# Performance work log

Measured on AMD Instinct MI355X. Metric: run time of the kernel, lower is better.

Reference implementation:

```python
import jax, jax.numpy as jnp
import numpy as np

EMBED_DIM = 1024
NUM_HEADS = 16
HEAD_DIM = EMBED_DIM // NUM_HEADS
SCALE = HEAD_DIM ** -0.5


def setup_inputs() -> dict:
    key = jax.random.key(0)
    ks = jax.random.split(key, 5)
    B, N, C = 4, 2048, EMBED_DIM
    s = C ** -0.5
    return {
        "x": jax.random.normal(ks[0], (B, N, C), dtype=jnp.float32),
        "w_qkv": jax.random.normal(ks[1], (C, 3 * C), dtype=jnp.float32) * s,
        "b_qkv": jnp.zeros((3 * C,), dtype=jnp.float32),
        "w_proj": jax.random.normal(ks[2], (C, C), dtype=jnp.float32) * s,
        "b_proj": jnp.zeros((C,), dtype=jnp.float32),
    }


def reference(x, w_qkv, b_qkv, w_proj, b_proj):
    B, N, C = x.shape
    H, D = NUM_HEADS, HEAD_DIM
    qkv = x @ w_qkv + b_qkv                      # (B, N, 3C)
    qkv = qkv.reshape(B, N, 3, H, D)
    qkv = jnp.transpose(qkv, (2, 0, 3, 1, 4))    # (3, B, H, N, D)
    q, k, v = qkv[0], qkv[1], qkv[2]
    attn = jnp.einsum('bhnd,bhmd->bhnm', q, k) * SCALE
    attn = jax.nn.softmax(attn, axis=-1)
    out = jnp.einsum('bhnm,bhmd->bhnd', attn, v)  # (B, H, N, D)
    out = jnp.transpose(out, (0, 2, 1, 3)).reshape(B, N, C)
    return out @ w_proj + b_proj
```

## Files before the change

### kernel.cpp

```cpp
#include <hip/hip_runtime.h>

typedef __attribute__((ext_vector_type(8))) short short8v;
typedef __attribute__((ext_vector_type(4))) short short4v;
typedef __attribute__((ext_vector_type(4))) float float4v;
typedef __attribute__((ext_vector_type(4))) unsigned short ushort4v;
typedef __attribute__((ext_vector_type(8))) unsigned short ushort8v;

#define GLOBAL_AS __attribute__((address_space(1)))
#define LDS_AS __attribute__((address_space(3)))

__device__ __forceinline__ void async_cp16(const void* g, void* l) {
  __builtin_amdgcn_global_load_lds((const GLOBAL_AS void*)g, (LDS_AS void*)l, 16, 0, 0);
}

__device__ __forceinline__ unsigned short f2bf(float f) {
  unsigned u = __float_as_uint(f);
  u += 0x7fffu + ((u >> 16) & 1u);
  return (unsigned short)(u >> 16);
}

#if defined(__HIP_DEVICE_COMPILE__)
#if __has_builtin(__builtin_amdgcn_exp2f)
#define EXP2F(x) __builtin_amdgcn_exp2f(x)
#else
#define EXP2F(x) exp2f(x)
#endif
#else
#define EXP2F(x) exp2f(x)
#endif

#if defined(__HIP_DEVICE_COMPILE__) && __has_builtin(__builtin_amdgcn_cvt_pk_bf16_f32)
typedef __attribute__((ext_vector_type(2))) __bf16 bf16x2v;
__device__ __forceinline__ unsigned pk_bf16(float a, float b) {
  bf16x2v r = __builtin_amdgcn_cvt_pk_bf16_f32(a, b);
  return __builtin_bit_cast(unsigned, r);
}
#else
__device__ __forceinline__ unsigned pk_bf16(float a, float b) {
  return (unsigned)f2bf(a) | ((unsigned)f2bf(b) << 16);
}
#endif

#define MFMA_QK(a, b, c) __builtin_amdgcn_mfma_f32_16x16x32_bf16(a, b, c, 0, 0, 0)


__global__ __launch_bounds__(256) void cvt_f32_bf16(const float* __restrict__ src,
                                                    unsigned short* __restrict__ dst) {
  int i = blockIdx.x * 256 + threadIdx.x;
  float4 v = ((const float4*)src)[i];
  ushort4v o;
  o.x = f2bf(v.x); o.y = f2bf(v.y); o.z = f2bf(v.z); o.w = f2bf(v.w);
  ((ushort4v*)dst)[i] = o;
}

__global__ __launch_bounds__(256) void transpose_w(const float* __restrict__ src,
                                                   unsigned short* __restrict__ dst,
                                                   int K, int N) {
  __shared__ float tile[64][65];
  int k0 = blockIdx.x * 64, n0 = blockIdx.y * 64;
  int t = threadIdx.x;
  int tc = t & 15, tr = t >> 4;
#pragma unroll
  for (int p = 0; p < 4; p++) {
    int r = tr + p * 16;
    float4 v = *(const float4*)(src + (size_t)(k0 + r) * N + n0 + tc * 4);
    tile[r][tc * 4 + 0] = v.x; tile[r][tc * 4 + 1] = v.y;
    tile[r][tc * 4 + 2] = v.z; tile[r][tc * 4 + 3] = v.w;
  }
  __syncthreads();
#pragma unroll
  for (int p = 0; p < 4; p++) {
    int rn = tr + p * 16;
    ushort4v o;
    o.x = f2bf(tile[tc * 4 + 0][rn]);
    o.y = f2bf(tile[tc * 4 + 1][rn]);
    o.z = f2bf(tile[tc * 4 + 2][rn]);
    o.w = f2bf(tile[tc * 4 + 3][rn]);
    *(ushort4v*)(dst + (size_t)(n0 + rn) * K + k0 + tc * 4) = o;
  }
}


__global__ __launch_bounds__(256) void gemm_qkv(const unsigned short* __restrict__ A,
                                                const unsigned short* __restrict__ BT,
                                                const float* __restrict__ bias,
                                                unsigned short* __restrict__ Qo,
                                                unsigned short* __restrict__ Ko,
                                                unsigned short* __restrict__ VTo) {
  __shared__ unsigned short As[128 * 32];
  __shared__ unsigned short Bs[128 * 32];
  int tid = threadIdx.x;
  int lane = tid & 63, w = tid >> 6, g = lane >> 4, c = lane & 15;
  int m0 = blockIdx.x * 128, n0 = blockIdx.y * 128;
  int wm = (w & 1) * 64, wn = (w >> 1) * 64;
  float4v acc[4][4] = {};

  for (int k0 = 0; k0 < 1024; k0 += 32) {
    __syncthreads();
#pragma unroll
    for (int p = 0; p < 2; p++) {
      int idx = p * 256 + tid;
      int row = idx >> 2, c8 = (idx & 3) * 8;
      async_cp16(A + (size_t)(m0 + row) * 1024 + k0 + c8, &As[idx * 8]);
      async_cp16(BT + (size_t)(n0 + row) * 1024 + k0 + c8, &Bs[idx * 8]);
    }
    __syncthreads();
    short8v af[4], bf[4];
#pragma unroll
    for (int i = 0; i < 4; i++)
      af[i] = *(const short8v*)(&As[(wm + i * 16 + c) * 32 + g * 8]);
#pragma unroll
    for (int j = 0; j < 4; j++)
      bf[j] = *(const short8v*)(&Bs[(wn + j * 16 + c) * 32 + g * 8]);
#pragma unroll
    for (int i = 0; i < 4; i++)
#pragma unroll
      for (int j = 0; j < 4; j++)
        acc[i][j] = MFMA_QK(af[i], bf[j], acc[i][j]);
  }

  int which = n0 >> 10;
#pragma unroll
  for (int j = 0; j < 4; j++) {
    int ng = n0 + wn + j * 16 + c;
    float bv = bias[ng];
    int h = (ng & 1023) >> 6, d = ng & 63;
#pragma unroll
    for (int i = 0; i < 4; i++) {
#pragma unroll
      for (int r = 0; r < 4; r++) {
        int mg = m0 + wm + i * 16 + g * 4 + r;
        int b = mg >> 11, n = mg & 2047;
        float v = acc[i][j][r] + bv;
        if (which == 0)
          Qo[((size_t)(b * 16 + h) * 2048 + n) * 64 + d] = f2bf(v * 0.18033688011112042f);
        else if (which == 1)
          Ko[((size_t)(b * 16 + h) * 2048 + n) * 64 + d] = f2bf(v);
        else
          VTo[((size_t)(b * 16 + h) * 64 + d) * 2048 + n] = f2bf(v);
      }
    }
  }
}


#define NTOK 2048
#define BK 64

__global__ __launch_bounds__(256, 4) void attn_kernel(const unsigned short* __restrict__ Qg,
                                                      const unsigned short* __restrict__ Kg,
                                                      const unsigned short* __restrict__ VTg,
                                                      unsigned short* __restrict__ Og) {
  __shared__ unsigned short Ks[2][BK * 64];
  __shared__ unsigned short VTs[2][64 * BK];

  int tid = threadIdx.x;
  int lane = tid & 63, w = tid >> 6, g = lane >> 4, c = lane & 15;
  int gh2 = g >> 1, g1 = g & 1;
  int id = blockIdx.x;
  int xcd = id & 7, within = id >> 3;
  int bh = xcd * 8 + (within >> 4);
  int q0 = (within & 15) * 128;

  const unsigned short* Qb = Qg + (size_t)bh * NTOK * 64;
  const unsigned short* Kb = Kg + (size_t)bh * NTOK * 64;
  const unsigned short* VTb = VTg + (size_t)bh * 64 * NTOK;

  short8v qf[2][2];
#pragma unroll
  for (int nt = 0; nt < 2; nt++)
#pragma unroll
    for (int kk = 0; kk < 2; kk++)
      qf[nt][kk] = *(const short8v*)(Qb + (size_t)(q0 + w * 32 + nt * 16 + c) * 64 +
                                     kk * 32 + g * 8);

  short8v ones8;
#pragma unroll
  for (int i = 0; i < 8; i++) ones8[i] = (short)0x3F80;

  float4v lacc[2] = {};
  float4v o[2][4] = {};

#pragma unroll
  for (int p = 0; p < 2; p++) {
    int idx = p * 256 + tid;
    int row = idx >> 3, ch = idx & 7;
    async_cp16(Kb + (size_t)row * 64 + ((ch ^ (row & 7)) * 8), &Ks[0][idx * 8]);
    async_cp16(VTb + (size_t)row * NTOK + ((ch ^ (row & 7)) * 8), &VTs[0][idx * 8]);
  }

  for (int it = 0; it < NTOK / BK; it++) {
    int pb = it & 1;
    __syncthreads();

    if (it + 1 < NTOK / BK) {
      int kt = (it + 1) * BK;
#pragma unroll
      for (int p = 0; p < 2; p++) {
        int idx = p * 256 + tid;
        int row = idx >> 3, ch = idx & 7;
        async_cp16(Kb + (size_t)(kt + row) * 64 + ((ch ^ (row & 7)) * 8),
                   &Ks[1 - pb][idx * 8]);
        async_cp16(VTb + (size_t)row * NTOK + kt + ((ch ^ (row & 7)) * 8),
                   &VTs[1 - pb][idx * 8]);
      }
    }

    const unsigned short* Kp = &Ks[pb][0];
    const unsigned short* Vp = &VTs[pb][0];

#pragma unroll
    for (int t = 0; t < 2; t++) {
      float4v st[2][2] = {};
#pragma unroll
      for (int mth = 0; mth < 2; mth++) {
        int row = (t * 2 + mth) * 16 + c;
        short8v kf[2];
#pragma unroll
        for (int kk = 0; kk < 2; kk++) {
          int ch = (kk * 4 + g) ^ (row & 7);
          kf[kk] = *(const short8v*)(Kp + row * 64 + ch * 8);
        }
#pragma unroll
        for (int nt = 0; nt < 2; nt++)
#pragma unroll
          for (int kk = 0; kk < 2; kk++)
            st[mth][nt] = MFMA_QK(kf[kk], qf[nt][kk], st[mth][nt]);
      }

      short8v pa8[2];
#pragma unroll
      for (int nt = 0; nt < 2; nt++) {
        float4v a = st[0][nt], b2 = st[1][nt];
        a.x = EXP2F(a.x); a.y = EXP2F(a.y); a.z = EXP2F(a.z); a.w = EXP2F(a.w);
        b2.x = EXP2F(b2.x); b2.y = EXP2F(b2.y); b2.z = EXP2F(b2.z); b2.w = EXP2F(b2.w);
        union { unsigned u[4]; short8v s; } cv;
        cv.u[0] = pk_bf16(a.x, a.y);
        cv.u[1] = pk_bf16(a.z, a.w);
        cv.u[2] = pk_bf16(b2.x, b2.y);
        cv.u[3] = pk_bf16(b2.z, b2.w);
        pa8[nt] = cv.s;
      }

#pragma unroll
      for (int nt_o = 0; nt_o < 4; nt_o++) {
        int d = nt_o * 16 + c;
        int s1 = (t * 4 + gh2) ^ (d & 7);
        int s2 = (t * 4 + 2 + gh2) ^ (d & 7);
        union { short4v h[2]; short8v s8; } vb;
        vb.h[0] = *(const short4v*)(Vp + d * BK + s1 * 8 + g1 * 4);
        vb.h[1] = *(const short4v*)(Vp + d * BK + s2 * 8 + g1 * 4);
#pragma unroll
        for (int mt_o = 0; mt_o < 2; mt_o++)
          o[mt_o][nt_o] = MFMA_QK(pa8[mt_o], vb.s8, o[mt_o][nt_o]);
      }
#pragma unroll
      for (int mt_o = 0; mt_o < 2; mt_o++)
        lacc[mt_o] = MFMA_QK(pa8[mt_o], ones8, lacc[mt_o]);
    }
  }

  int b = bh >> 4, h = bh & 15;
#pragma unroll
  for (int mt_o = 0; mt_o < 2; mt_o++) {
    float4v li;
#pragma unroll
    for (int r = 0; r < 4; r++) li[r] = 1.0f / lacc[mt_o][r];
#pragma unroll
    for (int nt_o = 0; nt_o < 4; nt_o++) {
      float4v v = o[mt_o][nt_o] * li;
      int col = h * 64 + nt_o * 16 + c;
      int rowbase = b * NTOK + q0 + w * 32 + mt_o * 16 + g * 4;
#pragma unroll
      for (int r = 0; r < 4; r++)
        Og[(size_t)(rowbase + r) * 1024 + col] = f2bf(v[r]);
    }
  }
}

__global__ __launch_bounds__(256) void gemm_proj(const unsigned short* __restrict__ A,
                                                 const unsigned short* __restrict__ BT,
                                                 const float* __restrict__ bias,
                                                 float* __restrict__ out) {
  __shared__ unsigned short As[128 * 32];
  __shared__ unsigned short Bs[128 * 32];
  int tid = threadIdx.x;
  int lane = tid & 63, w = tid >> 6, g = lane >> 4, c = lane & 15;
  int m0 = blockIdx.x * 128, n0 = blockIdx.y * 128;
  int wm = (w & 1) * 64, wn = (w >> 1) * 64;
  float4v acc[4][4] = {};

  for (int k0 = 0; k0 < 1024; k0 += 32) {
    __syncthreads();
#pragma unroll
    for (int p = 0; p < 2; p++) {
      int idx = p * 256 + tid;
      int row = idx >> 2, c8 = (idx & 3) * 8;
      async_cp16(A + (size_t)(m0 + row) * 1024 + k0 + c8, &As[idx * 8]);
      async_cp16(BT + (size_t)(n0 + row) * 1024 + k0 + c8, &Bs[idx * 8]);
    }
    __syncthreads();
    short8v af[4], bf[4];
#pragma unroll
    for (int i = 0; i < 4; i++)
      af[i] = *(const short8v*)(&As[(wm + i * 16 + c) * 32 + g * 8]);
#pragma unroll
    for (int j = 0; j < 4; j++)
      bf[j] = *(const short8v*)(&Bs[(wn + j * 16 + c) * 32 + g * 8]);
#pragma unroll
    for (int i = 0; i < 4; i++)
#pragma unroll
      for (int j = 0; j < 4; j++)
        acc[i][j] = MFMA_QK(af[i], bf[j], acc[i][j]);
  }

#pragma unroll
  for (int j = 0; j < 4; j++) {
    int ng = n0 + wn + j * 16 + c;
    float bv = bias[ng];
#pragma unroll
    for (int i = 0; i < 4; i++) {
#pragma unroll
      for (int r = 0; r < 4; r++) {
        int mg = m0 + wm + i * 16 + g * 4 + r;
        out[(size_t)mg * 1024 + ng] = acc[i][j][r] + bv;
      }
    }
  }
}


extern "C" void kernel_launch(void* const* d_in, const int* in_sizes, int n_in,
                              void* d_out, int out_size, void* d_ws, size_t ws_size,
                              hipStream_t stream) {
  (void)in_sizes; (void)n_in; (void)out_size; (void)ws_size;
  const float* x = (const float*)d_in[0];
  const float* w_qkv = (const float*)d_in[1];
  const float* b_qkv = (const float*)d_in[2];
  const float* w_proj = (const float*)d_in[3];
  const float* b_proj = (const float*)d_in[4];
  float* out = (float*)d_out;

  unsigned short* x_bf = (unsigned short*)d_ws;
  unsigned short* wqkvT = x_bf + (size_t)8192 * 1024;
  unsigned short* wprojT = wqkvT + (size_t)3072 * 1024;
  unsigned short* qws = wprojT + (size_t)1024 * 1024;
  unsigned short* kws = qws + (size_t)8388608;
  unsigned short* vtws = kws + (size_t)8388608;
  unsigned short* aws = vtws + (size_t)8388608;

  cvt_f32_bf16<<<8192, 256, 0, stream>>>(x, x_bf);
  transpose_w<<<dim3(16, 48), 256, 0, stream>>>(w_qkv, wqkvT, 1024, 3072);
  transpose_w<<<dim3(16, 16), 256, 0, stream>>>(w_proj, wprojT, 1024, 1024);
  gemm_qkv<<<dim3(64, 24), 256, 0, stream>>>(x_bf, wqkvT, b_qkv, qws, kws, vtws);
  attn_kernel<<<1024, 256, 0, stream>>>(qws, kws, vtws, aws);
  gemm_proj<<<dim3(64, 8), 256, 0, stream>>>(aws, wprojT, b_proj, out);
}
```

Before: 298.4 us.

## Double attention query tile per wave and permute V layout for single-load fragments

Each wave now handles 64 query rows instead of 32, so every K and V fragment read from LDS feeds twice as many MFMAs. The grid is halved to 512 blocks and the occupancy hint drops to 2 blocks per CU to make room for the larger accumulators. The QKV GEMM now writes V-transpose with a permuted token order within each 32-token group, so one 16-byte LDS load produces a B fragment instead of two 8-byte loads. s_setprio is raised around the MFMA sections to favour matrix work over the exp phase. The costs are higher register pressure and lower occupancy, which reduces latency hiding.

```diff
diff --git a/kernel.cpp b/kernel.cpp
--- a/kernel.cpp
+++ b/kernel.cpp
@@ -136,8 +136,10 @@
           Qo[((size_t)(b * 16 + h) * 2048 + n) * 64 + d] = f2bf(v * 0.18033688011112042f);
         else if (which == 1)
           Ko[((size_t)(b * 16 + h) * 2048 + n) * 64 + d] = f2bf(v);
-        else
-          VTo[((size_t)(b * 16 + h) * 64 + d) * 2048 + n] = f2bf(v);
+        else {
+          int np = (n & ~31) | (((n >> 2) & 3) << 3) | (((n >> 4) & 1) << 2) | (n & 3);
+          VTo[((size_t)(b * 16 + h) * 64 + d) * 2048 + np] = f2bf(v);
+        }
       }
     }
   }
@@ -147,7 +149,7 @@
 #define NTOK 2048
 #define BK 64
 
-__global__ __launch_bounds__(256, 4) void attn_kernel(const unsigned short* __restrict__ Qg,
+__global__ __launch_bounds__(256, 2) void attn_kernel(const unsigned short* __restrict__ Qg,
                                                       const unsigned short* __restrict__ Kg,
                                                       const unsigned short* __restrict__ VTg,
                                                       unsigned short* __restrict__ Og) {
@@ -156,30 +158,29 @@
 
   int tid = threadIdx.x;
   int lane = tid & 63, w = tid >> 6, g = lane >> 4, c = lane & 15;
-  int gh2 = g >> 1, g1 = g & 1;
   int id = blockIdx.x;
   int xcd = id & 7, within = id >> 3;
-  int bh = xcd * 8 + (within >> 4);
-  int q0 = (within & 15) * 128;
+  int bh = xcd * 8 + (within >> 3);
+  int q0 = (within & 7) * 256;
 
   const unsigned short* Qb = Qg + (size_t)bh * NTOK * 64;
   const unsigned short* Kb = Kg + (size_t)bh * NTOK * 64;
   const unsigned short* VTb = VTg + (size_t)bh * 64 * NTOK;
 
-  short8v qf[2][2];
-#pragma unroll
-  for (int nt = 0; nt < 2; nt++)
+  short8v qf[4][2];
+#pragma unroll
+  for (int nt = 0; nt < 4; nt++)
 #pragma unroll
     for (int kk = 0; kk < 2; kk++)
-      qf[nt][kk] = *(const short8v*)(Qb + (size_t)(q0 + w * 32 + nt * 16 + c) * 64 +
+      qf[nt][kk] = *(const short8v*)(Qb + (size_t)(q0 + w * 64 + nt * 16 + c) * 64 +
                                      kk * 32 + g * 8);
 
   short8v ones8;
 #pragma unroll
   for (int i = 0; i < 8; i++) ones8[i] = (short)0x3F80;
 
-  float4v lacc[2] = {};
-  float4v o[2][4] = {};
+  float4v lacc[4] = {};
+  float4v o[4][4] = {};
 
 #pragma unroll
   for (int p = 0; p < 2; p++) {
@@ -211,7 +212,8 @@
 
 #pragma unroll
     for (int t = 0; t < 2; t++) {
-      float4v st[2][2] = {};
+      float4v st[2][4] = {};
+      __builtin_amdgcn_s_setprio(1);
 #pragma unroll
       for (int mth = 0; mth < 2; mth++) {
         int row = (t * 2 + mth) * 16 + c;
@@ -222,15 +224,16 @@
           kf[kk] = *(const short8v*)(Kp + row * 64 + ch * 8);
         }
 #pragma unroll
-        for (int nt = 0; nt < 2; nt++)
+        for (int nt = 0; nt < 4; nt++)
 #pragma unroll
           for (int kk = 0; kk < 2; kk++)
             st[mth][nt] = MFMA_QK(kf[kk], qf[nt][kk], st[mth][nt]);
       }
-
-      short8v pa8[2];
-#pragma unroll
-      for (int nt = 0; nt < 2; nt++) {
+      __builtin_amdgcn_s_setprio(0);
+
+      short8v pa8[4];
+#pragma unroll
+      for (int nt = 0; nt < 4; nt++) {
         float4v a = st[0][nt], b2 = st[1][nt];
         a.x = EXP2F(a.x); a.y = EXP2F(a.y); a.z = EXP2F(a.z); a.w = EXP2F(a.w);
         b2.x = EXP2F(b2.x); b2.y = EXP2F(b2.y); b2.z = EXP2F(b2.z); b2.w = EXP2F(b2.w);
@@ -242,35 +245,34 @@
         pa8[nt] = cv.s;
       }
 
+      __builtin_amdgcn_s_setprio(1);
 #pragma unroll
       for (int nt_o = 0; nt_o < 4; nt_o++) {
         int d = nt_o * 16 + c;
-        int s1 = (t * 4 + gh2) ^ (d & 7);
-        int s2 = (t * 4 + 2 + gh2) ^ (d & 7);
-        union { short4v h[2]; short8v s8; } vb;
-        vb.h[0] = *(const short4v*)(Vp + d * BK + s1 * 8 + g1 * 4);
-        vb.h[1] = *(const short4v*)(Vp + d * BK + s2 * 8 + g1 * 4);
-#pragma unroll
-        for (int mt_o = 0; mt_o < 2; mt_o++)
-          o[mt_o][nt_o] = MFMA_QK(pa8[mt_o], vb.s8, o[mt_o][nt_o]);
-      }
-#pragma unroll
-      for (int mt_o = 0; mt_o < 2; mt_o++)
-        lacc[mt_o] = MFMA_QK(pa8[mt_o], ones8, lacc[mt_o]);
+        int s = (t * 4 + g) ^ (d & 7);
+        short8v vb8 = *(const short8v*)(Vp + d * BK + s * 8);
+#pragma unroll
+        for (int mt = 0; mt < 4; mt++)
+          o[mt][nt_o] = MFMA_QK(pa8[mt], vb8, o[mt][nt_o]);
+      }
+#pragma unroll
+      for (int mt = 0; mt < 4; mt++)
+        lacc[mt] = MFMA_QK(pa8[mt], ones8, lacc[mt]);
+      __builtin_amdgcn_s_setprio(0);
     }
   }
 
   int b = bh >> 4, h = bh & 15;
 #pragma unroll
-  for (int mt_o = 0; mt_o < 2; mt_o++) {
+  for (int mt = 0; mt < 4; mt++) {
     float4v li;
 #pragma unroll
-    for (int r = 0; r < 4; r++) li[r] = 1.0f / lacc[mt_o][r];
+    for (int r = 0; r < 4; r++) li[r] = 1.0f / lacc[mt][r];
 #pragma unroll
     for (int nt_o = 0; nt_o < 4; nt_o++) {
-      float4v v = o[mt_o][nt_o] * li;
+      float4v v = o[mt][nt_o] * li;
       int col = h * 64 + nt_o * 16 + c;
-      int rowbase = b * NTOK + q0 + w * 32 + mt_o * 16 + g * 4;
+      int rowbase = b * NTOK + q0 + w * 64 + mt * 16 + g * 4;
 #pragma unroll
       for (int r = 0; r < 4; r++)
         Og[(size_t)(rowbase + r) * 1024 + col] = f2bf(v[r]);
@@ -353,6 +355,6 @@
   transpose_w<<<dim3(16, 48), 256, 0, stream>>>(w_qkv, wqkvT, 1024, 3072);
   transpose_w<<<dim3(16, 16), 256, 0, stream>>>(w_proj, wprojT, 1024, 1024);
   gemm_qkv<<<dim3(64, 24), 256, 0, stream>>>(x_bf, wqkvT, b_qkv, qws, kws, vtws);
-  attn_kernel<<<1024, 256, 0, stream>>>(qws, kws, vtws, aws);
+  attn_kernel<<<512, 256, 0, stream>>>(qws, kws, vtws, aws);
   gemm_proj<<<dim3(64, 8), 256, 0, stream>>>(aws, wprojT, b_proj, out);
 }
```

New measurement: 294.9 us. Within noise of the previous version (-1.2%).
